# Kernel tuning notes

Hardware: AMD Instinct MI355X
Metric: run time of the kernel (lower is better)

Reference implementation:

```python
import jax, jax.numpy as jnp
import numpy as np

PATCH = 64      # patch_size
K = 16          # num_patches
UNF_K = 16      # unfold kernel
UNF_S = 8       # unfold stride


def setup_inputs() -> dict:
    key = jax.random.key(0)
    k0, k1, k2 = jax.random.split(key, 3)
    B, C, H, W = 32, 3, 384, 384
    x = jax.random.normal(k0, (B, C, H, W), dtype=jnp.float32)
    # encoder params: Conv2d(3,32,3,s2,p1) -> ReLU -> Conv2d(32,64,3,s2,p1) -> GAP
    w1 = jax.random.normal(k1, (32, 3, 3, 3), dtype=jnp.float32) * 0.1
    b1 = jnp.zeros((32,), dtype=jnp.float32)
    w2 = jax.random.normal(k2, (64, 32, 3, 3), dtype=jnp.float32) * 0.05
    b2 = jnp.zeros((64,), dtype=jnp.float32)
    return {"x": x, "w1": w1, "b1": b1, "w2": w2, "b2": b2}


def _patch_variances(x):
    # torch.var(unfold(x,16,8), dim=1), unbiased, over C*16*16 = 768 elems.
    # Computed via window sums instead of materializing the unfold tensor.
    win = (1, 1, UNF_K, UNF_K)
    st = (1, 1, UNF_S, UNF_S)
    s = jax.lax.reduce_window(x, 0.0, jax.lax.add, win, st, 'VALID')
    s2 = jax.lax.reduce_window(x * x, 0.0, jax.lax.add, win, st, 'VALID')
    s = s.sum(axis=1)    # [B, gh, gw]
    s2 = s2.sum(axis=1)  # [B, gh, gw]
    n = x.shape[1] * UNF_K * UNF_K  # 768
    var = (s2 - s * s / n) / (n - 1)
    return var.reshape(var.shape[0], -1)  # [B, gh*gw], row-major like F.unfold


def _encode(patches, w1, b1, w2, b2):
    # patches: [N, 3, 64, 64] -> [N, 64]
    dn = ('NCHW', 'OIHW', 'NCHW')
    y = jax.lax.conv_general_dilated(patches, w1, (2, 2), [(1, 1), (1, 1)],
                                     dimension_numbers=dn) + b1[None, :, None, None]
    y = jax.nn.relu(y)
    y = jax.lax.conv_general_dilated(y, w2, (2, 2), [(1, 1), (1, 1)],
                                     dimension_numbers=dn) + b2[None, :, None, None]
    return y.mean(axis=(2, 3))  # AdaptiveAvgPool2d(1)


def reference(x, w1, b1, w2, b2):
    B, C, H, W = x.shape
    var = _patch_variances(x)                 # [B, L]
    _, idx = jax.lax.top_k(var, K)            # [B, K]
    # faithful (buggy) decode from the source: divisor is W//8, step 8
    h = (idx // (W // UNF_S)) * UNF_S         # [B, K]
    w = (idx % (W // UNF_S)) * UNF_S          # [B, K]

    def slice_one(img, hh, ww):
        # dynamic_slice clamps starts so the 64x64 crop stays in-bounds
        return jax.lax.dynamic_slice(img, (0, hh, ww), (C, PATCH, PATCH))

    gather = jax.vmap(lambda img, hs, ws: jax.vmap(
        lambda hh, ww: slice_one(img, hh, ww))(hs, ws))
    patches = gather(x, h, w)                 # [B, K, 3, 64, 64]
    feats = _encode(patches.reshape(B * K, C, PATCH, PATCH), w1, b1, w2, b2)
    return feats.reshape(B, K, -1).mean(axis=1)  # [B, 64]
```

## Files before the change

kernel.cpp:

```cpp
#include <hip/hip_runtime.h>
#include <math.h>

#define NB 32
#define GH 47
#define GW 47
#define NWIN (GH*GW)
#define KSEL 16
#define RPITCH 17
#define SEG 48

__global__ __launch_bounds__(256) void k_var(const float* __restrict__ x,
                                             float* __restrict__ var)
{
    __shared__ double hs [3][24][SEG];
    __shared__ double hs2[3][24][SEG];
    int gyp = blockIdx.x;
    int b   = blockIdx.y;
    int tid = threadIdx.x;
    int R0  = gyp * 16;

    for (int tau = tid; tau < 3*24*SEG; tau += 256) {
        int sg = tau % SEG;
        int t2 = tau / SEG;
        int rr = t2 % 24;
        int c  = t2 / 24;
        int row = R0 + rr;
        double s = 0.0, s2 = 0.0;
        if (row < 384) {
            const float* px = x + (((size_t)(b*3 + c)*384 + row)*384 + sg*8);
            #pragma unroll
            for (int q = 0; q < 2; ++q) {
                float4 v = *reinterpret_cast<const float4*>(px + q*4);
                double a0 = v.x, a1 = v.y, a2 = v.z, a3 = v.w;
                s  += a0 + a1 + a2 + a3;
                s2 = fma(a0,a0, fma(a1,a1, fma(a2,a2, fma(a3,a3, s2))));
            }
        }
        hs [c][rr][sg] = s;
        hs2[c][rr][sg] = s2;
    }
    __syncthreads();

    if (tid < 188) {
        int which = tid & 1;
        int rest  = tid >> 1;
        int gx = rest % 47, g = rest / 47;
        int gy = gyp*2 + g;
        if (gy < GH) {
            const double* base = which ? &hs2[0][0][0] : &hs[0][0][0];
            double S = 0.0;
            #pragma unroll
            for (int c = 0; c < 3; ++c)
                #pragma unroll
                for (int r = 0; r < 16; ++r) {
                    const double* rp = base + ((c*24) + (g*8 + r))*SEG + gx;
                    S += rp[0] + rp[1];
                }
            double P = __shfl_xor(S, 1, 64);
            if (which == 0) {
                var[(size_t)b*NWIN + gy*GW + gx] =
                    (float)((P - S*S/768.0) / 767.0);
            }
        }
    }
}

__global__ __launch_bounds__(256) void k_topk(const float* __restrict__ var,
                                              int* __restrict__ coords)
{
    __shared__ float lv[NWIN];
    __shared__ float s_val[4];
    __shared__ int   s_idx[4];
    __shared__ int   chosen[KSEL];
    int b = blockIdx.x, tid = threadIdx.x;
    int lane = tid & 63, wavid = tid >> 6;

    for (int i = tid; i < NWIN; i += 256) lv[i] = var[(size_t)b*NWIN + i];
    __syncthreads();

    for (int k = 0; k < KSEL; ++k) {
        float bv = -INFINITY; int bi = NWIN;
        for (int i = tid; i < NWIN; i += 256) {
            float v = lv[i];
            if (v > bv) { bv = v; bi = i; }
        }
        #pragma unroll
        for (int m = 1; m < 64; m <<= 1) {
            float ov = __shfl_xor(bv, m, 64);
            int   oi = __shfl_xor(bi, m, 64);
            if (ov > bv || (ov == bv && oi < bi)) { bv = ov; bi = oi; }
        }
        if (lane == 0) { s_val[wavid] = bv; s_idx[wavid] = bi; }
        __syncthreads();
        if (tid == 0) {
            float cv = s_val[0]; int ci = s_idx[0];
            #pragma unroll
            for (int wv = 1; wv < 4; ++wv) {
                if (s_val[wv] > cv || (s_val[wv] == cv && s_idx[wv] < ci)) {
                    cv = s_val[wv]; ci = s_idx[wv];
                }
            }
            chosen[k] = ci;
            lv[ci] = -INFINITY;
        }
        __syncthreads();
    }

    if (tid < KSEL) {
        int idx = chosen[tid];
        int h = (idx / 48) * 8; if (h > 320) h = 320;
        int w = (idx % 48) * 8; if (w > 320) w = 320;
        coords[(b*KSEL + tid)*2 + 0] = h;
        coords[(b*KSEL + tid)*2 + 1] = w;
    }
}

__global__ __launch_bounds__(1024, 1) void k_encode(const float* __restrict__ x,
    const float* __restrict__ w1, const float* __restrict__ b1,
    const int* __restrict__ coords, float* __restrict__ sbuf)
{
    __shared__ float4 sin4[3*66*RPITCH];
    __shared__ float4 w1t4[27*8];
    __shared__ float4 b1t4[8];
    __shared__ float  s_part[16][2][4][3];
    __shared__ float  s_c31[8][4][3];

    int p    = blockIdx.x;
    int bimg = p >> 4;
    int tid  = threadIdx.x;
    int h0 = coords[p*2 + 0];
    int w0 = coords[p*2 + 1];

    float* sinf = (float*)sin4;
    float* w1tf = (float*)w1t4;
    float* b1tf = (float*)b1t4;

    if (tid < 896) {
        if (tid < 864) w1tf[tid] = w1[(tid & 31)*27 + (tid >> 5)];
        else           b1tf[tid - 864] = b1[tid - 864];
    }

    if (tid < 243) {
        int c = tid / 81, j = tid - c*81;
        if (j < 17) {
            sin4[(c*66 + 0)*RPITCH + j] = make_float4(0.f, 0.f, 0.f, 0.f);
        } else {
            int r  = j - 16;
            int sw = (r >> 1) & 7;
            sinf[((c*66 + r)*RPITCH + sw)*4] = 0.f;
        }
    }

    #pragma unroll
    for (int it = 0; it < 3; ++it) {
        int fi  = tid + it*1024;
        int c   = fi >> 10;
        int rem = fi & 1023;
        int y   = rem >> 4;
        int x4  = rem & 15;
        float4 v = *reinterpret_cast<const float4*>(
            x + (((size_t)(bimg*3 + c)*384 + (h0 + y))*384 + w0 + x4*4));
        int r  = y + 1;
        int sw = (r >> 1) & 7;
        float vals[4] = {v.x, v.y, v.z, v.w};
        #pragma unroll
        for (int e = 0; e < 4; ++e) {
            int pcol = x4*4 + 1 + e;
            int k  = pcol >> 2, bb = pcol & 3;
            int ks = (k < 16) ? ((k & 8) | ((k & 7) ^ sw)) : 16;
            sinf[((c*66 + r)*RPITCH + ks)*4 + bb] = vals[e];
        }
    }
    __syncthreads();

    int wave = tid >> 6;
    int lane = tid & 63;
    int sub  = wave & 1;
    int icq  = __builtin_amdgcn_readfirstlane(tid >> 7);
    int iy   = sub*16 + (lane >> 2);
    int xq   = lane & 3;

    float acc[4][8];
    #pragma unroll
    for (int i = 0; i < 4; ++i)
        #pragma unroll
        for (int u = 0; u < 8; ++u) acc[i][u] = 0.f;

    #pragma unroll 1
    for (int ch = 0; ch < 3; ++ch) {
        #pragma unroll 1
        for (int ky = 0; ky < 3; ++ky) {
            int widx = ch*9 + ky*3;
            float4 wv0 = w1t4[(widx + 0)*8 + icq];
            float4 wv1 = w1t4[(widx + 1)*8 + icq];
            float4 wv2 = w1t4[(widx + 2)*8 + icq];
            const float* pw0 = (const float*)&wv0;
            const float* pw1 = (const float*)&wv1;
            const float* pw2 = (const float*)&wv2;

            int r    = 2*iy + ky;
            int sw   = (r >> 1) & 7;
            int base = (ch*66 + r)*RPITCH;
            float s[17];
            #pragma unroll
            for (int j = 0; j < 4; ++j) {
                int k = 4*xq + j;
                float4 v = sin4[base + ((k & 8) | ((k & 7) ^ sw))];
                s[4*j+0] = v.x; s[4*j+1] = v.y; s[4*j+2] = v.z; s[4*j+3] = v.w;
            }
            {
                int k  = 4*xq + 4;
                int ks = (k < 16) ? ((k & 8) | ((k & 7) ^ sw)) : 16;
                s[16] = sinf[(base + ks)*4];
            }
            #pragma unroll
            for (int i = 0; i < 4; ++i) {
                #pragma unroll
                for (int u = 0; u < 8; ++u)
                    acc[i][u] = fmaf(s[2*u], pw0[i],
                                 fmaf(s[2*u+1], pw1[i],
                                  fmaf(s[2*u+2], pw2[i], acc[i][u])));
            }
        }
    }

    float4 bv = b1t4[icq];
    const float* pb = (const float*)&bv;
    float R[4][3];
    #pragma unroll
    for (int i = 0; i < 4; ++i) {
        float bias = pb[i];
        float c1 = 0.f, c2 = 0.f, v7 = 0.f;
        #pragma unroll
        for (int u = 0; u < 8; ++u) {
            float v = fmaxf(acc[i][u] + bias, 0.f);
            if (u & 1) c2 += v; else c1 += v;
            if (u == 7) v7 = v;
        }
        R[i][0] = c2 - ((xq == 3) ? v7 : 0.f);
        R[i][1] = c1;
        R[i][2] = c2;
    }

    #pragma unroll
    for (int m = 1; m <= 2; m <<= 1)
        #pragma unroll
        for (int i = 0; i < 4; ++i)
            #pragma unroll
            for (int k = 0; k < 3; ++k)
                R[i][k] += __shfl_xor(R[i][k], m, 64);

    float c31[4][3];
    #pragma unroll
    for (int i = 0; i < 4; ++i)
        #pragma unroll
        for (int k = 0; k < 3; ++k)
            c31[i][k] = __shfl(R[i][k], 60, 64);

    #pragma unroll
    for (int m = 8; m < 64; m <<= 1)
        #pragma unroll
        for (int i = 0; i < 4; ++i)
            #pragma unroll
            for (int k = 0; k < 3; ++k)
                R[i][k] += __shfl_xor(R[i][k], m, 64);

    if (lane == 0) {
        #pragma unroll
        for (int i = 0; i < 4; ++i)
            #pragma unroll
            for (int k = 0; k < 3; ++k)
                s_part[wave][0][i][k] = R[i][k];
    } else if (lane == 4) {
        #pragma unroll
        for (int i = 0; i < 4; ++i)
            #pragma unroll
            for (int k = 0; k < 3; ++k)
                s_part[wave][1][i][k] = R[i][k];
    }
    if (sub == 1 && lane == 8) {
        #pragma unroll
        for (int i = 0; i < 4; ++i)
            #pragma unroll
            for (int k = 0; k < 3; ++k)
                s_c31[icq][i][k] = c31[i][k];
    }
    __syncthreads();

    if (tid < 288) {
        int ic = tid / 9, j = tid - ic*9;
        int ky = j / 3, kx = j - ky*3;
        int g = ic >> 2, i = ic & 3;
        float even = s_part[2*g][0][i][kx] + s_part[2*g+1][0][i][kx];
        float odd  = s_part[2*g][1][i][kx] + s_part[2*g+1][1][i][kx];
        float val = (ky == 1) ? even : odd;
        if (ky == 0) val = odd - s_c31[g][i][kx];
        sbuf[(size_t)p*288 + tid] = val;
    }
}

__global__ __launch_bounds__(256) void k_reduce(const float* __restrict__ sbuf,
    const float* __restrict__ w2, const float* __restrict__ b2,
    float* __restrict__ out)
{
    __shared__ float Ssum[288];
    __shared__ float s_part[256];
    int b = blockIdx.x, tid = threadIdx.x;

    for (int i = tid; i < 288; i += 256) {
        float s = 0.f;
        #pragma unroll
        for (int k = 0; k < KSEL; ++k)
            s += sbuf[(size_t)(b*KSEL + k)*288 + i];
        Ssum[i] = s;
    }
    __syncthreads();

    int oc = tid & 63, q = tid >> 6;
    const float4* w4 = reinterpret_cast<const float4*>(w2 + oc*288 + q*72);
    const float4* S4 = reinterpret_cast<const float4*>(Ssum + q*72);
    float a = 0.f;
    #pragma unroll
    for (int t = 0; t < 18; ++t) {
        float4 wv = w4[t];
        float4 sv = S4[t];
        a = fmaf(wv.x, sv.x, fmaf(wv.y, sv.y,
             fmaf(wv.z, sv.z, fmaf(wv.w, sv.w, a))));
    }
    s_part[tid] = a;
    __syncthreads();
    if (tid < 64) {
        float t = s_part[tid] + s_part[64 + tid] + s_part[128 + tid] + s_part[192 + tid];
        out[b*64 + tid] = b2[tid] + t * (1.0f/4096.0f);
    }
}

extern "C" void kernel_launch(void* const* d_in, const int* in_sizes, int n_in,
                              void* d_out, int out_size, void* d_ws, size_t ws_size,
                              hipStream_t stream)
{
    const float* x  = (const float*)d_in[0];
    const float* w1 = (const float*)d_in[1];
    const float* b1 = (const float*)d_in[2];
    const float* w2 = (const float*)d_in[3];
    const float* b2 = (const float*)d_in[4];
    float* out = (float*)d_out;

    char* ws = (char*)d_ws;
    int*   coords = (int*)ws;
    float* var    = (float*)(ws + 4096);
    float* sbuf   = (float*)(ws + 287744);

    k_var   <<<dim3(24, NB), 256, 0, stream>>>(x, var);
    k_topk  <<<NB,           256, 0, stream>>>(var, coords);
    k_encode<<<NB*KSEL,     1024, 0, stream>>>(x, w1, b1, coords, sbuf);
    k_reduce<<<NB,           256, 0, stream>>>(sbuf, w2, b2, out);
}
```

Before: 79.45 us.

## Fuse top-k selection into encode kernel with redundant per-block argmax

Removes the separate top-k kernel launch. Each encode block now loads its image's variance map into shared memory and runs iterative argmax until it reaches its own rank. The argmax packs an order-preserving float key and the index into one 64-bit key, so each reduction step is a single max. This drops one launch and the round trip of coordinates through global memory, at the cost of every one of the 16 blocks per image repeating up to 16 argmax passes and adding shared-memory pressure.

After: 85.85 us. 8.1% more time.

```diff
diff --git a/kernel.cpp b/kernel.cpp
--- a/kernel.cpp
+++ b/kernel.cpp
@@ -65,81 +65,40 @@
     }
 }
 
-__global__ __launch_bounds__(256) void k_topk(const float* __restrict__ var,
-                                              int* __restrict__ coords)
-{
-    __shared__ float lv[NWIN];
-    __shared__ float s_val[4];
-    __shared__ int   s_idx[4];
-    __shared__ int   chosen[KSEL];
-    int b = blockIdx.x, tid = threadIdx.x;
-    int lane = tid & 63, wavid = tid >> 6;
-
-    for (int i = tid; i < NWIN; i += 256) lv[i] = var[(size_t)b*NWIN + i];
-    __syncthreads();
-
-    for (int k = 0; k < KSEL; ++k) {
-        float bv = -INFINITY; int bi = NWIN;
-        for (int i = tid; i < NWIN; i += 256) {
-            float v = lv[i];
-            if (v > bv) { bv = v; bi = i; }
-        }
-        #pragma unroll
-        for (int m = 1; m < 64; m <<= 1) {
-            float ov = __shfl_xor(bv, m, 64);
-            int   oi = __shfl_xor(bi, m, 64);
-            if (ov > bv || (ov == bv && oi < bi)) { bv = ov; bi = oi; }
-        }
-        if (lane == 0) { s_val[wavid] = bv; s_idx[wavid] = bi; }
-        __syncthreads();
-        if (tid == 0) {
-            float cv = s_val[0]; int ci = s_idx[0];
-            #pragma unroll
-            for (int wv = 1; wv < 4; ++wv) {
-                if (s_val[wv] > cv || (s_val[wv] == cv && s_idx[wv] < ci)) {
-                    cv = s_val[wv]; ci = s_idx[wv];
-                }
-            }
-            chosen[k] = ci;
-            lv[ci] = -INFINITY;
-        }
-        __syncthreads();
-    }
-
-    if (tid < KSEL) {
-        int idx = chosen[tid];
-        int h = (idx / 48) * 8; if (h > 320) h = 320;
-        int w = (idx % 48) * 8; if (w > 320) w = 320;
-        coords[(b*KSEL + tid)*2 + 0] = h;
-        coords[(b*KSEL + tid)*2 + 1] = w;
-    }
-}
-
 __global__ __launch_bounds__(1024, 1) void k_encode(const float* __restrict__ x,
     const float* __restrict__ w1, const float* __restrict__ b1,
-    const int* __restrict__ coords, float* __restrict__ sbuf)
+    const float* __restrict__ var, float* __restrict__ sbuf)
 {
     __shared__ float4 sin4[3*66*RPITCH];
+    __shared__ float  lv[NWIN];
     __shared__ float4 w1t4[27*8];
     __shared__ float4 b1t4[8];
+    __shared__ unsigned long long s_red[16];
     __shared__ float  s_part[16][2][4][3];
     __shared__ float  s_c31[8][4][3];
-
-    int p    = blockIdx.x;
-    int bimg = p >> 4;
-    int tid  = threadIdx.x;
-    int h0 = coords[p*2 + 0];
-    int w0 = coords[p*2 + 1];
+    __shared__ int    s_hw[2];
+
+    int p     = blockIdx.x;
+    int bimg  = p >> 4;
+    int krank = p & 15;
+    int tid   = threadIdx.x;
+    int wave  = tid >> 6;
+    int lane  = tid & 63;
 
     float* sinf = (float*)sin4;
     float* w1tf = (float*)w1t4;
     float* b1tf = (float*)b1t4;
 
+    {
+        const float* vb = var + (size_t)bimg*NWIN;
+        lv[tid] = vb[tid];
+        lv[tid + 1024] = vb[tid + 1024];
+        if (tid < NWIN - 2048) lv[tid + 2048] = vb[tid + 2048];
+    }
     if (tid < 896) {
         if (tid < 864) w1tf[tid] = w1[(tid & 31)*27 + (tid >> 5)];
         else           b1tf[tid - 864] = b1[tid - 864];
     }
-
     if (tid < 243) {
         int c = tid / 81, j = tid - c*81;
         if (j < 17) {
@@ -150,6 +109,59 @@
             sinf[((c*66 + r)*RPITCH + sw)*4] = 0.f;
         }
     }
+    __syncthreads();
+
+    for (int it = 0; ; ++it) {
+        unsigned long long bk = 0ULL;
+        {
+            unsigned u0 = __float_as_uint(lv[tid]);
+            unsigned m0 = u0 ^ ((unsigned)((int)u0 >> 31) | 0x80000000u);
+            unsigned long long k0 =
+                ((unsigned long long)m0 << 12) | (unsigned)(4095 - tid);
+            unsigned u1 = __float_as_uint(lv[tid + 1024]);
+            unsigned m1 = u1 ^ ((unsigned)((int)u1 >> 31) | 0x80000000u);
+            unsigned long long k1 =
+                ((unsigned long long)m1 << 12) | (unsigned)(4095 - (tid + 1024));
+            bk = k0 > k1 ? k0 : k1;
+            if (tid < NWIN - 2048) {
+                unsigned u2 = __float_as_uint(lv[tid + 2048]);
+                unsigned m2 = u2 ^ ((unsigned)((int)u2 >> 31) | 0x80000000u);
+                unsigned long long k2 =
+                    ((unsigned long long)m2 << 12) | (unsigned)(4095 - (tid + 2048));
+                bk = k2 > bk ? k2 : bk;
+            }
+        }
+        #pragma unroll
+        for (int m = 1; m < 64; m <<= 1) {
+            unsigned long long o = __shfl_xor(bk, m, 64);
+            bk = o > bk ? o : bk;
+        }
+        if (lane == 0) s_red[wave] = bk;
+        __syncthreads();
+        if (wave == 0) {
+            unsigned long long v = (lane < 16) ? s_red[lane] : 0ULL;
+            #pragma unroll
+            for (int m = 1; m < 16; m <<= 1) {
+                unsigned long long o = __shfl_xor(v, m, 64);
+                v = o > v ? o : v;
+            }
+            if (lane == 0) {
+                int idx = 4095 - (int)(v & 0xFFFULL);
+                if (it == krank) {
+                    int h = (idx / 48) * 8; if (h > 320) h = 320;
+                    int w = (idx % 48) * 8; if (w > 320) w = 320;
+                    s_hw[0] = h; s_hw[1] = w;
+                } else {
+                    lv[idx] = -INFINITY;
+                }
+            }
+        }
+        __syncthreads();
+        if (it == krank) break;
+    }
+
+    int h0 = s_hw[0];
+    int w0 = s_hw[1];
 
     #pragma unroll
     for (int it = 0; it < 3; ++it) {
@@ -173,8 +185,6 @@
     }
     __syncthreads();
 
-    int wave = tid >> 6;
-    int lane = tid & 63;
     int sub  = wave & 1;
     int icq  = __builtin_amdgcn_readfirstlane(tid >> 7);
     int iy   = sub*16 + (lane >> 2);
@@ -347,12 +357,10 @@
     float* out = (float*)d_out;
 
     char* ws = (char*)d_ws;
-    int*   coords = (int*)ws;
-    float* var    = (float*)(ws + 4096);
-    float* sbuf   = (float*)(ws + 287744);
+    float* var  = (float*)ws;
+    float* sbuf = (float*)(ws + 283904);
 
     k_var   <<<dim3(24, NB), 256, 0, stream>>>(x, var);
-    k_topk  <<<NB,           256, 0, stream>>>(var, coords);
-    k_encode<<<NB*KSEL,     1024, 0, stream>>>(x, w1, b1, coords, sbuf);
+    k_encode<<<NB*KSEL,     1024, 0, stream>>>(x, w1, b1, var, sbuf);
     k_reduce<<<NB,           256, 0, stream>>>(sbuf, w2, b2, out);
 }
```

## Split each patch encode across two half-height blocks of 512 threads

Applied to the files above, without the earlier changes.

The encode kernel now launches two blocks per selected patch, each handling 32 output rows of conv1 with 512 threads and a half-sized shared input tile. Per-block partial sums go to separate sbuf slots, and the reduce kernel sums 32 partials per image instead of 16. This aims to improve occupancy and latency hiding (two blocks per CU, smaller LDS footprint, more blocks to schedule). The cost is a one-row halo reload, twice the partial writes, and a heavier reduction read.

New measurement: 77.81 us. 1.02x faster.

```diff
diff --git a/kernel.cpp b/kernel.cpp
--- a/kernel.cpp
+++ b/kernel.cpp
@@ -115,17 +115,18 @@
     }
 }
 
-__global__ __launch_bounds__(1024, 1) void k_encode(const float* __restrict__ x,
+__global__ __launch_bounds__(512, 2) void k_encode(const float* __restrict__ x,
     const float* __restrict__ w1, const float* __restrict__ b1,
     const int* __restrict__ coords, float* __restrict__ sbuf)
 {
-    __shared__ float4 sin4[3*66*RPITCH];
+    __shared__ float4 sin4[3*33*RPITCH];
     __shared__ float4 w1t4[27*8];
-    __shared__ float4 b1t4[8];
-    __shared__ float  s_part[16][2][4][3];
+    __shared__ float  s_part[8][2][4][3];
     __shared__ float  s_c31[8][4][3];
 
-    int p    = blockIdx.x;
+    int bid  = blockIdx.x;
+    int p    = bid >> 1;
+    int grp  = bid & 1;
     int bimg = p >> 4;
     int tid  = threadIdx.x;
     int h0 = coords[p*2 + 0];
@@ -133,51 +134,52 @@
 
     float* sinf = (float*)sin4;
     float* w1tf = (float*)w1t4;
-    float* b1tf = (float*)b1t4;
-
-    if (tid < 896) {
-        if (tid < 864) w1tf[tid] = w1[(tid & 31)*27 + (tid >> 5)];
-        else           b1tf[tid - 864] = b1[tid - 864];
-    }
-
-    if (tid < 243) {
-        int c = tid / 81, j = tid - c*81;
-        if (j < 17) {
-            sin4[(c*66 + 0)*RPITCH + j] = make_float4(0.f, 0.f, 0.f, 0.f);
-        } else {
-            int r  = j - 16;
-            int sw = (r >> 1) & 7;
-            sinf[((c*66 + r)*RPITCH + sw)*4] = 0.f;
-        }
-    }
-
-    #pragma unroll
-    for (int it = 0; it < 3; ++it) {
-        int fi  = tid + it*1024;
-        int c   = fi >> 10;
-        int rem = fi & 1023;
-        int y   = rem >> 4;
-        int x4  = rem & 15;
-        float4 v = *reinterpret_cast<const float4*>(
-            x + (((size_t)(bimg*3 + c)*384 + (h0 + y))*384 + w0 + x4*4));
-        int r  = y + 1;
-        int sw = (r >> 1) & 7;
-        float vals[4] = {v.x, v.y, v.z, v.w};
-        #pragma unroll
-        for (int e = 0; e < 4; ++e) {
-            int pcol = x4*4 + 1 + e;
-            int k  = pcol >> 2, bb = pcol & 3;
-            int ks = (k < 16) ? ((k & 8) | ((k & 7) ^ sw)) : 16;
-            sinf[((c*66 + r)*RPITCH + ks)*4 + bb] = vals[e];
+
+    for (int i = tid; i < 864; i += 512)
+        w1tf[i] = w1[(i & 31)*27 + (i >> 5)];
+
+    if (tid < 150) {
+        if (tid < 99) {
+            int c = tid / 33, lr = tid - c*33;
+            int sw = (lr >> 1) & 7;
+            sinf[((c*33 + lr)*RPITCH + sw)*4] = 0.f;
+        } else if (grp == 0) {
+            int j = tid - 99;
+            int c = j / 17, f4i = j - c*17;
+            sin4[(c*33 + 0)*RPITCH + f4i] = make_float4(0.f, 0.f, 0.f, 0.f);
+        }
+    }
+
+    #pragma unroll
+    for (int it = 0; it < 4; ++it) {
+        int fi = tid + it*512;
+        if (fi < 3*33*16) {
+            int c   = fi / 528;
+            int rem = fi - c*528;
+            int lr  = rem >> 4;
+            int x4  = rem & 15;
+            int y   = 32*grp + lr - 1;
+            if (y >= 0) {
+                float4 v = *reinterpret_cast<const float4*>(
+                    x + (((size_t)(bimg*3 + c)*384 + (h0 + y))*384 + w0 + x4*4));
+                int sw = (lr >> 1) & 7;
+                float vals[4] = {v.x, v.y, v.z, v.w};
+                #pragma unroll
+                for (int e = 0; e < 4; ++e) {
+                    int pcol = x4*4 + 1 + e;
+                    int k  = pcol >> 2, bb = pcol & 3;
+                    int ks = (k < 16) ? ((k & 8) | ((k & 7) ^ sw)) : 16;
+                    sinf[((c*33 + lr)*RPITCH + ks)*4 + bb] = vals[e];
+                }
+            }
         }
     }
     __syncthreads();
 
     int wave = tid >> 6;
     int lane = tid & 63;
-    int sub  = wave & 1;
-    int icq  = __builtin_amdgcn_readfirstlane(tid >> 7);
-    int iy   = sub*16 + (lane >> 2);
+    int icq  = __builtin_amdgcn_readfirstlane(wave);
+    int iyl  = lane >> 2;
     int xq   = lane & 3;
 
     float acc[4][8];
@@ -198,9 +200,9 @@
             const float* pw1 = (const float*)&wv1;
             const float* pw2 = (const float*)&wv2;
 
-            int r    = 2*iy + ky;
-            int sw   = (r >> 1) & 7;
-            int base = (ch*66 + r)*RPITCH;
+            int lr   = 2*iyl + ky;
+            int sw   = (lr >> 1) & 7;
+            int base = (ch*33 + lr)*RPITCH;
             float s[17];
             #pragma unroll
             for (int j = 0; j < 4; ++j) {
@@ -224,12 +226,10 @@
         }
     }
 
-    float4 bv = b1t4[icq];
-    const float* pb = (const float*)&bv;
     float R[4][3];
     #pragma unroll
     for (int i = 0; i < 4; ++i) {
-        float bias = pb[i];
+        float bias = b1[icq*4 + i];
         float c1 = 0.f, c2 = 0.f, v7 = 0.f;
         #pragma unroll
         for (int u = 0; u < 8; ++u) {
@@ -277,25 +277,24 @@
             #pragma unroll
             for (int k = 0; k < 3; ++k)
                 s_part[wave][1][i][k] = R[i][k];
-    }
-    if (sub == 1 && lane == 8) {
-        #pragma unroll
-        for (int i = 0; i < 4; ++i)
-            #pragma unroll
-            for (int k = 0; k < 3; ++k)
-                s_c31[icq][i][k] = c31[i][k];
+    } else if (lane == 8) {
+        #pragma unroll
+        for (int i = 0; i < 4; ++i)
+            #pragma unroll
+            for (int k = 0; k < 3; ++k)
+                s_c31[wave][i][k] = c31[i][k];
     }
     __syncthreads();
 
     if (tid < 288) {
         int ic = tid / 9, j = tid - ic*9;
         int ky = j / 3, kx = j - ky*3;
-        int g = ic >> 2, i = ic & 3;
-        float even = s_part[2*g][0][i][kx] + s_part[2*g+1][0][i][kx];
-        float odd  = s_part[2*g][1][i][kx] + s_part[2*g+1][1][i][kx];
+        int q = ic >> 2, i = ic & 3;
+        float even = s_part[q][0][i][kx];
+        float odd  = s_part[q][1][i][kx];
         float val = (ky == 1) ? even : odd;
-        if (ky == 0) val = odd - s_c31[g][i][kx];
-        sbuf[(size_t)p*288 + tid] = val;
+        if (ky == 0 && grp == 1) val = odd - s_c31[q][i][kx];
+        sbuf[(size_t)bid*288 + tid] = val;
     }
 }
 
@@ -310,8 +309,8 @@
     for (int i = tid; i < 288; i += 256) {
         float s = 0.f;
         #pragma unroll
-        for (int k = 0; k < KSEL; ++k)
-            s += sbuf[(size_t)(b*KSEL + k)*288 + i];
+        for (int k = 0; k < 2*KSEL; ++k)
+            s += sbuf[(size_t)(b*2*KSEL + k)*288 + i];
         Ssum[i] = s;
     }
     __syncthreads();
@@ -351,8 +350,8 @@
     float* var    = (float*)(ws + 4096);
     float* sbuf   = (float*)(ws + 287744);
 
-    k_var   <<<dim3(24, NB), 256, 0, stream>>>(x, var);
-    k_topk  <<<NB,           256, 0, stream>>>(var, coords);
-    k_encode<<<NB*KSEL,     1024, 0, stream>>>(x, w1, b1, coords, sbuf);
-    k_reduce<<<NB,           256, 0, stream>>>(sbuf, w2, b2, out);
-}
+    k_var   <<<dim3(24, NB),  256, 0, stream>>>(x, var);
+    k_topk  <<<NB,            256, 0, stream>>>(var, coords);
+    k_encode<<<NB*KSEL*2,     512, 0, stream>>>(x, w1, b1, coords, sbuf);
+    k_reduce<<<NB,            256, 0, stream>>>(sbuf, w2, b2, out);
+}
```
